# Kernel tuning notes

Measured on AMD Instinct MI355X. Metric: run time of the kernel, lower is better.

Reference implementation:

```python
import jax, jax.numpy as jnp
import numpy as np
import math

B, S, H, NH = 8, 1024, 1024, 16
DH = H // NH


def _ln(x, g, b, eps=1e-5):
    m = x.mean(-1, keepdims=True)
    v = ((x - m) ** 2).mean(-1, keepdims=True)
    return (x - m) / jnp.sqrt(v + eps) * g + b


def _attn(qx, kx, vx, wq, bq, wk, bk, wv, bv, wo, bo, mask):
    b = qx.shape[0]
    def heads(t, w, bias):
        return (t @ w + bias).reshape(b, -1, NH, DH).transpose(0, 2, 1, 3)
    q, k, v = heads(qx, wq, bq), heads(kx, wk, bk), heads(vx, wv, bv)
    corr = jnp.einsum('bhqd,bhkd->bhqk', q, k) / math.sqrt(DH)  # [B,NH,Sq,Sk]
    corr = jnp.where(mask[:, None, :, None] == 0, -1e9, corr)  # mask per query row
    p = jax.nn.softmax(corr, axis=-1)
    o = jnp.einsum('bhqk,bhkd->bhqd', p, v).transpose(0, 2, 1, 3).reshape(b, -1, H)
    return o @ wo + bo


def setup_inputs() -> dict:
    key = jax.random.key(0)
    ks = jax.random.split(key, 16)
    d = {}
    d['x'] = jax.random.normal(ks[0], (B, S, H), jnp.float32)
    d['h'] = jax.random.normal(ks[1], (B, S, H), jnp.float32)
    d['mask'] = jnp.ones((B, S), jnp.int32)
    wnames = ['sa_wq', 'sa_wk', 'sa_wv', 'sa_wo', 'ca_wq', 'ca_wk', 'ca_wv', 'ca_wo', 'ff_w1', 'ff_w2']
    for i, n in enumerate(wnames):
        d[n] = jax.random.normal(ks[2 + i], (H, H), jnp.float32) * 0.02
    for n in ['sa_bq', 'sa_bk', 'sa_bv', 'sa_bo', 'ca_bq', 'ca_bk', 'ca_bv', 'ca_bo', 'ff_b1', 'ff_b2']:
        d[n] = jnp.zeros((H,), jnp.float32)
    for n in ['ln1', 'ln2', 'ln3', 'lnh', 'ff_ln']:
        d[n + '_g'] = jnp.ones((H,), jnp.float32)
        d[n + '_b'] = jnp.zeros((H,), jnp.float32)
    return d


def reference(x, h, mask, ln1_g, ln1_b, ln2_g, ln2_b, ln3_g, ln3_b, lnh_g, lnh_b,
              sa_wq, sa_bq, sa_wk, sa_bk, sa_wv, sa_bv, sa_wo, sa_bo,
              ca_wq, ca_bq, ca_wk, ca_bk, ca_wv, ca_bv, ca_wo, ca_bo,
              ff_w1, ff_b1, ff_w2, ff_b2, ff_ln_g, ff_ln_b):
    # self-attention block (pre-LN, residual)
    xn = _ln(x, ln1_g, ln1_b)
    hidden_in = _attn(xn, xn, xn, sa_wq, sa_bq, sa_wk, sa_bk, sa_wv, sa_bv, sa_wo, sa_bo, mask) + x
    # cross-attention block
    mid_n = _ln(hidden_in, ln2_g, ln2_b)
    hn = _ln(h, lnh_g, lnh_b)
    hidden_mid = _attn(mid_n, hn, hn, ca_wq, ca_bq, ca_wk, ca_bk, ca_wv, ca_bv, ca_wo, ca_bo, mask) + hidden_in
    # position-wise FFN (Conv1d k=1 == pointwise linear) with its own LN+residual
    y = _ln(hidden_mid, ln3_g, ln3_b)
    ff = jax.nn.relu(y @ ff_w1 + ff_b1) @ ff_w2 + ff_b2
    ffo = _ln(ff + y, ff_ln_g, ff_ln_b)
    return ffo + hidden_mid
```

## Files before the change

kernel.cpp:

```cpp
#include <hip/hip_runtime.h>

typedef unsigned short u16;
typedef unsigned int u32;
typedef float f32x4 __attribute__((ext_vector_type(4)));
typedef float f32x16 __attribute__((ext_vector_type(16)));
typedef __bf16 bf16x8 __attribute__((ext_vector_type(8)));

#define MFMA16(a, b, c) __builtin_amdgcn_mfma_f32_16x16x32_bf16(a, b, c, 0, 0, 0)
#define MFMA32(a, b, c) __builtin_amdgcn_mfma_f32_32x32x16_bf16(a, b, c, 0, 0, 0)
#define PLSWAP(x, y) asm volatile("v_permlane32_swap_b32 %0, %1" : "+v"(x), "+v"(y))
#define CFENCE() asm volatile("" ::: "memory")
#define BAR()                         \
    {                                 \
        CFENCE();                     \
        __builtin_amdgcn_s_barrier(); \
        CFENCE();                     \
    }
#define WAITV(n) asm volatile("s_waitcnt vmcnt(" #n ")" ::: "memory")

__device__ __forceinline__ u16 f2b(float f) {
    u32 u = __builtin_bit_cast(u32, f);
    u += 0x7fffu + ((u >> 16) & 1u);
    return (u16)(u >> 16);
}

__device__ __forceinline__ u32 pk2(float a, float b) {
    union { u32 u; __bf16 h[2]; } r;
    r.h[0] = (__bf16)a; r.h[1] = (__bf16)b;
    return r.u;
}

__device__ __forceinline__ void gload16(const u16* g, u16* l) {
    __builtin_amdgcn_global_load_lds((const __attribute__((address_space(1))) void*)g,
                                     (__attribute__((address_space(3))) void*)l, 16, 0, 0);
}

struct W10 { const float* p[10]; };
__global__ __launch_bounds__(256) void tcvt_k(W10 wp, u16* __restrict__ WT0) {
    const float* __restrict__ Wm = wp.p[blockIdx.z];
    u16* __restrict__ WT = WT0 + (size_t)blockIdx.z * 1048576;
    __shared__ float t[32][33];
    int bx = blockIdx.x, by = blockIdx.y;
    int tx = threadIdx.x, ty = threadIdx.y;
#pragma unroll
    for (int j = 0; j < 32; j += 8)
        t[ty + j][tx] = Wm[(size_t)(by * 32 + ty + j) * 1024 + bx * 32 + tx];
    __syncthreads();
#pragma unroll
    for (int j = 0; j < 32; j += 8)
        WT[(size_t)(bx * 32 + ty + j) * 1024 + by * 32 + tx] = f2b(t[tx][ty + j]);
}

__global__ __launch_bounds__(256) void vtr_k(const u16* __restrict__ Vg, int ldv, u16* __restrict__ VT) {
    __shared__ u16 t[32][34];
    int bx = blockIdx.x, by = blockIdx.y, b = blockIdx.z;
    int tx = threadIdx.x, ty = threadIdx.y;
#pragma unroll
    for (int j = 0; j < 32; j += 8)
        t[ty + j][tx] = Vg[(size_t)(b * 1024 + by * 32 + ty + j) * ldv + bx * 32 + tx];
    __syncthreads();
#pragma unroll
    for (int j = 0; j < 32; j += 8)
        VT[(size_t)(b * 1024 + bx * 32 + ty + j) * 1024 + by * 32 + tx] = t[tx][ty + j];
}

template <int MODE>
__global__ __launch_bounds__(256) void ln_k(const float* __restrict__ in1, const float* __restrict__ in2,
                                            const float* __restrict__ gg, const float* __restrict__ bb,
                                            const float* __restrict__ post,
                                            float* __restrict__ of, u16* __restrict__ ob) {
    int row = blockIdx.x, tid = threadIdx.x;
    size_t base = (size_t)row * 1024 + tid * 4;
    float4 x = *(const float4*)(in1 + base);
    if constexpr (MODE & 1) {
        float4 x2 = *(const float4*)(in2 + base);
        x.x += x2.x; x.y += x2.y; x.z += x2.z; x.w += x2.w;
    }
    float s1 = x.x + x.y + x.z + x.w;
    float s2 = x.x * x.x + x.y * x.y + x.z * x.z + x.w * x.w;
#pragma unroll
    for (int m = 32; m >= 1; m >>= 1) { s1 += __shfl_xor(s1, m); s2 += __shfl_xor(s2, m); }
    __shared__ float r1[4], r2[4];
    int lane = tid & 63, w = tid >> 6;
    if (lane == 0) { r1[w] = s1; r2[w] = s2; }
    __syncthreads();
    s1 = r1[0] + r1[1] + r1[2] + r1[3];
    s2 = r2[0] + r2[1] + r2[2] + r2[3];
    float mean = s1 * (1.0f / 1024.0f);
    float var = s2 * (1.0f / 1024.0f) - mean * mean;
    float rstd = rsqrtf(var + 1e-5f);
    float4 gv = *(const float4*)(gg + tid * 4);
    float4 bv = *(const float4*)(bb + tid * 4);
    float y0 = (x.x - mean) * rstd * gv.x + bv.x;
    float y1 = (x.y - mean) * rstd * gv.y + bv.y;
    float y2 = (x.z - mean) * rstd * gv.z + bv.z;
    float y3 = (x.w - mean) * rstd * gv.w + bv.w;
    if constexpr (MODE & 2) {
        float o0 = y0, o1 = y1, o2 = y2, o3 = y3;
        if constexpr (MODE & 8) {
            float4 p = *(const float4*)(post + base);
            o0 += p.x; o1 += p.y; o2 += p.z; o3 += p.w;
        }
        float4 o; o.x = o0; o.y = o1; o.z = o2; o.w = o3;
        *(float4*)(of + base) = o;
    }
    if constexpr (MODE & 4) {
        uint2 pk;
        pk.x = (u32)f2b(y0) | ((u32)f2b(y1) << 16);
        pk.y = (u32)f2b(y2) | ((u32)f2b(y3) << 16);
        *(uint2*)(ob + base) = pk;
    }
}

template <int EPI, int NBT>
__global__ __launch_bounds__(256, 2) void gemm_k(const u16* __restrict__ A, int lda,
                                                 const u16* __restrict__ WT,
                                                 const float* __restrict__ b0, const float* __restrict__ b1,
                                                 const float* __restrict__ b2,
                                                 float sc0, float sc1, float sc2,
                                                 const float* __restrict__ res,
                                                 void* __restrict__ outp, int ldc) {
    __shared__ u16 lds[32768];
    int id = blockIdx.x;
    const int CPX = 64 * NBT / 8;
    int swz = (id & 7) * CPX + (id >> 3);
    int bm = swz / NBT, bn = swz % NBT;
    const int m0 = bm * 128, n0 = bn * 128;
    int tid = threadIdx.x, lane = tid & 63, w = tid >> 6;
    int wm = w >> 1, wn = w & 1;
    int col = lane & 15, fg = lane >> 4;

    int r = tid >> 2, g = tid & 3;
    int gr = r ^ ((r >> 3) & 1);
    int gg = g ^ ((r >> 1) & 3);
    const u16* Asrc = A + (size_t)(m0 + gr) * lda + gg * 8;
    const u16* Bsrc = WT + (size_t)(n0 + gr) * 1024 + gg * 8;
    u16* aDst = lds + w * 512;
    u16* bDst = lds + 16384 + w * 512;

#define STG(slot, kt)                                                      \
    {                                                                      \
        gload16(Asrc + (kt) * 32, aDst + (slot) * 4096);                   \
        gload16(Asrc + (kt) * 32 + (size_t)64 * lda, aDst + (slot) * 4096 + 2048); \
        gload16(Bsrc + (kt) * 32, bDst + (slot) * 4096);                   \
        gload16(Bsrc + (kt) * 32 + (size_t)64 * 1024, bDst + (slot) * 4096 + 2048); \
    }

    int aoff = (((wm * 64 + col) * 32) + fg * 8) ^ ((col >> 1) << 3);
    int boff = (((wn * 64 + col) * 32) + fg * 8) ^ ((col >> 1) << 3);

    f32x4 acc[4][4];
#pragma unroll
    for (int m = 0; m < 4; m++)
#pragma unroll
        for (int n = 0; n < 4; n++) acc[m][n] = (f32x4){0.f, 0.f, 0.f, 0.f};

    auto body = [&](int slot) {
        const u16* aS = lds + slot * 4096;
        const u16* bS = lds + 16384 + slot * 4096;
        bf16x8 af[4], bfv[4];
#pragma unroll
        for (int m = 0; m < 4; m++) af[m] = *(const bf16x8*)(aS + aoff + m * 512);
#pragma unroll
        for (int n = 0; n < 4; n++) bfv[n] = *(const bf16x8*)(bS + boff + n * 512);
        __builtin_amdgcn_s_setprio(1);
#pragma unroll
        for (int m = 0; m < 4; m++)
#pragma unroll
            for (int n = 0; n < 4; n++) acc[m][n] = MFMA16(af[m], bfv[n], acc[m][n]);
        __builtin_amdgcn_s_setprio(0);
    };

    STG(0, 0); STG(1, 1); STG(2, 2);
#pragma unroll 4
    for (int s = 0; s < 29; ++s) {
        STG((s + 3) & 3, s + 3);
        WAITV(12);
        BAR();
        body(s & 3);
        BAR();
    }
    WAITV(8);  BAR(); body(1); BAR();
    WAITV(4);  BAR(); body(2); BAR();
    WAITV(0);  BAR(); body(3); BAR();
#undef STG

    int seg = n0 >> 10;
    const float* bp = (NBT == 8) ? b0 : (seg == 0 ? b0 : (seg == 1 ? b1 : b2));
    float sg = (NBT == 8) ? sc0 : (seg == 0 ? sc0 : (seg == 1 ? sc1 : sc2));
    int nseg = n0 & 1023;
    float bv[4];
#pragma unroll
    for (int n = 0; n < 4; n++) bv[n] = bp[nseg + wn * 64 + n * 16 + col];
#pragma unroll
    for (int m = 0; m < 4; m++) {
#pragma unroll
        for (int rr = 0; rr < 4; rr++) {
            int row = m0 + wm * 64 + m * 16 + fg * 4 + rr;
#pragma unroll
            for (int n = 0; n < 4; n++) {
                int c = n0 + wn * 64 + n * 16 + col;
                size_t idx = (size_t)row * ldc + c;
                float v = (acc[m][n][rr] + bv[n]) * sg;
                if constexpr (EPI == 0) ((u16*)outp)[idx] = f2b(v);
                else if constexpr (EPI == 1) ((u16*)outp)[idx] = f2b(fmaxf(v, 0.f));
                else if constexpr (EPI == 2) ((float*)outp)[idx] = v + res[idx];
            }
        }
    }
}

__global__ __launch_bounds__(256) void attn_k(const u16* __restrict__ Q, int ldq,
                                              const u16* __restrict__ Kc, int ldk,
                                              const u16* __restrict__ VT,
                                              const int* __restrict__ mask,
                                              u16* __restrict__ O, int ldo) {
    const int S = 1024;
    int gid = blockIdx.x;
    int bq = gid >> 7, hh = (gid >> 3) & 15, bb = gid & 7;
    int tid = threadIdx.x, lane = tid & 63, w = tid >> 6;
    int q = lane & 31, hl = lane >> 5;
    int q0w = bq * 128 + w * 32;

    __shared__ u16 sm[18432];
#define KT(b, r, c) sm[(b) * 9216 + (r) * 72 + (c)]
#define VTL(b, r, c) sm[(b) * 9216 + 4608 + (r) * 72 + (c)]

    const u16* Qrow = Q + ((size_t)bb * S + q0w + q) * ldq + hh * 64;
    bool mneg = (mask[bb * S + q0w + q] == 0);
    bf16x8 qf[4];
#pragma unroll
    for (int c = 0; c < 4; c++) {
        qf[c] = *(const bf16x8*)(Qrow + c * 16 + hl * 8);
        if (mneg) qf[c] = (bf16x8)(__bf16)0.f;
    }

    float l = 0.f;
    f32x16 oa[2];
#pragma unroll
    for (int i = 0; i < 16; i++) { oa[0][i] = 0.f; oa[1][i] = 0.f; }

    int kk = tid >> 2, ks = tid & 3;
    const u16* gK = Kc + ((size_t)bb * S + kk) * ldk + hh * 64 + ks * 16;
    const u16* gVT = VT + ((size_t)(bb * 16 + hh) * 64 + kk) * 1024 + ks * 16;
    uint4 kr0, kr1, vr0, vr1;

#define LOADT(t)                                                      \
    {                                                                 \
        const u16* pk_ = gK + (size_t)(t) * 64 * ldk;                 \
        kr0 = *(const uint4*)pk_; kr1 = *(const uint4*)(pk_ + 8);     \
        const u16* pv_ = gVT + (size_t)(t) * 64;                      \
        vr0 = *(const uint4*)pv_; vr1 = *(const uint4*)(pv_ + 8);     \
    }
#define STORET(bf)                                       \
    {                                                    \
        *(uint4*)&KT(bf, kk, ks * 16) = kr0;             \
        *(uint4*)&KT(bf, kk, ks * 16 + 8) = kr1;         \
        *(uint4*)&VTL(bf, kk, ks * 16) = vr0;            \
        *(uint4*)&VTL(bf, kk, ks * 16 + 8) = vr1;        \
    }

    LOADT(0);
    STORET(0);

    for (int t = 0; t < 16; ++t) {
        int cur = t & 1;
        if (t < 15) LOADT(t + 1);
        __syncthreads();

        f32x16 sc[2];
#pragma unroll
        for (int i = 0; i < 16; i++) { sc[0][i] = 0.f; sc[1][i] = 0.f; }
        __builtin_amdgcn_s_setprio(1);
#pragma unroll
        for (int st = 0; st < 2; st++)
#pragma unroll
            for (int c = 0; c < 4; c++) {
                bf16x8 kf = *(const bf16x8*)&KT(cur, st * 32 + q, c * 16 + hl * 8);
                sc[st] = MFMA32(kf, qf[c], sc[st]);
            }
        __builtin_amdgcn_s_setprio(0);

#pragma unroll
        for (int st = 0; st < 2; st++)
#pragma unroll
            for (int rr = 0; rr < 16; rr++) sc[st][rr] = exp2f(sc[st][rr]);
        float ts[8];
#pragma unroll
        for (int i = 0; i < 8; i++)
            ts[i] = (sc[0][i] + sc[0][i + 8]) + (sc[1][i] + sc[1][i + 8]);
#pragma unroll
        for (int i = 0; i < 4; i++) ts[i] += ts[i + 4];
        float rs = (ts[0] + ts[2]) + (ts[1] + ts[3]);
        rs += __shfl_xor(rs, 32);
        l += rs;

        __builtin_amdgcn_s_setprio(1);
#pragma unroll
        for (int st = 0; st < 2; st++) {
            u32 wv[8];
#pragma unroll
            for (int j = 0; j < 8; j++) wv[j] = pk2(sc[st][2 * j], sc[st][2 * j + 1]);
            PLSWAP(wv[0], wv[2]); PLSWAP(wv[1], wv[3]);
            PLSWAP(wv[4], wv[6]); PLSWAP(wv[5], wv[7]);
#pragma unroll
            for (int c = 0; c < 2; c++) {
                union { u32 u[4]; bf16x8 v; } pb;
                pb.u[0] = wv[c * 4 + 0]; pb.u[1] = wv[c * 4 + 1];
                pb.u[2] = wv[c * 4 + 2]; pb.u[3] = wv[c * 4 + 3];
#pragma unroll
                for (int dd = 0; dd < 2; dd++) {
                    bf16x8 vf = *(const bf16x8*)&VTL(cur, dd * 32 + q, st * 32 + c * 16 + hl * 8);
                    oa[dd] = MFMA32(vf, pb.v, oa[dd]);
                }
            }
        }
        __builtin_amdgcn_s_setprio(0);

        if (t < 15) STORET(cur ^ 1);
    }

    __syncthreads();
    float inv = 1.0f / l;
    u16* otw = sm + w * 2304;
#pragma unroll
    for (int dd = 0; dd < 2; dd++)
#pragma unroll
        for (int rr = 0; rr < 16; rr++) {
            int d = (rr & 3) + 8 * (rr >> 2) + 4 * hl + 32 * dd;
            otw[q * 72 + d] = f2b(oa[dd][rr] * inv);
        }
    __syncthreads();
    size_t obase = ((size_t)bb * S + q0w) * ldo + hh * 64;
#pragma unroll
    for (int i = 0; i < 4; i++) {
        int row = i * 8 + (lane >> 3);
        uint4 vdat = *(const uint4*)&otw[row * 72 + (lane & 7) * 8];
        *(uint4*)(O + obase + (size_t)row * ldo + (lane & 7) * 8) = vdat;
    }
#undef KT
#undef VTL
#undef LOADT
#undef STORET
}

extern "C" void kernel_launch(void* const* d_in, const int* in_sizes, int n_in,
                              void* d_out, int out_size, void* d_ws, size_t ws_size,
                              hipStream_t stream) {
    (void)in_sizes; (void)n_in; (void)out_size; (void)ws_size;
    const float* x = (const float*)d_in[0];
    const float* h = (const float*)d_in[1];
    const int* mask = (const int*)d_in[2];
    const float* W[10];
    const float* Bv[10];
    for (int i = 0; i < 10; i++) { W[i] = (const float*)d_in[3 + i]; Bv[i] = (const float*)d_in[13 + i]; }
    const float *ln1g = (const float*)d_in[23], *ln1b = (const float*)d_in[24];
    const float *ln2g = (const float*)d_in[25], *ln2b = (const float*)d_in[26];
    const float *ln3g = (const float*)d_in[27], *ln3b = (const float*)d_in[28];
    const float *lnhg = (const float*)d_in[29], *lnhb = (const float*)d_in[30];
    const float *flng = (const float*)d_in[31], *flnb = (const float*)d_in[32];

    const float SCLE = 0.18033688011112042f;

    char* ws = (char*)d_ws;
    size_t off = 0;
    auto alloc = [&](size_t bytes) -> char* {
        char* p = ws + off;
        off += (bytes + 255) & ~(size_t)255;
        return p;
    };
    const size_t MT = (size_t)8192 * 1024;
    u16* wtb = (u16*)alloc((size_t)10 * 1048576 * 2);
    u16* wt[10];
    for (int i = 0; i < 10; i++) wt[i] = wtb + (size_t)i * 1048576;
    u16* qkv = (u16*)alloc((size_t)8192 * 3072 * 2);
    u16* kv = qkv;
    u16* kb = qkv + (size_t)8192 * 2048;
    u16* bufA = (u16*)alloc(MT * 2);
    u16* qb   = (u16*)alloc(MT * 2);
    float* hid_in  = (float*)alloc(MT * 4);
    float* hid_mid = (float*)alloc(MT * 4);
    float* yf      = (float*)alloc(MT * 4);
    u16* hn = (u16*)yf;
    u16* vt_sa = bufA;
    u16* vt_ca = (u16*)hid_mid;
    float* outF = (float*)d_out;

    W10 wp;
    for (int i = 0; i < 10; i++) wp.p[i] = W[i];
    tcvt_k<<<dim3(32, 32, 10), dim3(32, 8), 0, stream>>>(wp, wtb);

    ln_k<4><<<8192, 256, 0, stream>>>(x, nullptr, ln1g, ln1b, nullptr, nullptr, bufA);
    gemm_k<0, 24><<<1536, 256, 0, stream>>>(bufA, 1024, wt[0], Bv[0], Bv[1], Bv[2], SCLE, 1.f, 1.f, nullptr, qkv, 3072);
    vtr_k<<<dim3(32, 32, 8), dim3(32, 8), 0, stream>>>(qkv + 2048, 3072, vt_sa);
    attn_k<<<1024, 256, 0, stream>>>(qkv, 3072, qkv + 1024, 3072, vt_sa, mask, qkv, 3072);
    gemm_k<2, 8><<<512, 256, 0, stream>>>(qkv, 3072, wt[3], Bv[3], Bv[3], Bv[3], 1.f, 1.f, 1.f, x, hid_in, 1024);

    ln_k<4><<<8192, 256, 0, stream>>>(hid_in, nullptr, ln2g, ln2b, nullptr, nullptr, bufA);
    ln_k<4><<<8192, 256, 0, stream>>>(h, nullptr, lnhg, lnhb, nullptr, nullptr, hn);
    gemm_k<0, 8><<<512, 256, 0, stream>>>(bufA, 1024, wt[4], Bv[4], Bv[4], Bv[4], SCLE, 1.f, 1.f, nullptr, qb, 1024);
    gemm_k<0, 16><<<1024, 256, 0, stream>>>(hn, 1024, wt[5], Bv[5], Bv[6], Bv[6], 1.f, 1.f, 1.f, nullptr, kv, 2048);
    vtr_k<<<dim3(32, 32, 8), dim3(32, 8), 0, stream>>>(kv + 1024, 2048, vt_ca);
    attn_k<<<1024, 256, 0, stream>>>(qb, 1024, kv, 2048, vt_ca, mask, qb, 1024);
    gemm_k<2, 8><<<512, 256, 0, stream>>>(qb, 1024, wt[7], Bv[7], Bv[7], Bv[7], 1.f, 1.f, 1.f, hid_in, hid_mid, 1024);

    ln_k<6><<<8192, 256, 0, stream>>>(hid_mid, nullptr, ln3g, ln3b, nullptr, yf, bufA);
    gemm_k<1, 8><<<512, 256, 0, stream>>>(bufA, 1024, wt[8], Bv[8], Bv[8], Bv[8], 1.f, 1.f, 1.f, nullptr, kb, 1024);
    gemm_k<2, 8><<<512, 256, 0, stream>>>(kb, 1024, wt[9], Bv[9], Bv[9], Bv[9], 1.f, 1.f, 1.f, yf, hid_in, 1024);
    ln_k<10><<<8192, 256, 0, stream>>>(hid_in, nullptr, flng, flnb, hid_mid, outF, nullptr);
}
```

Before: 511.9 us.

## Enlarge GEMM tiles to 256-row blocks with 8 waves and split-phase pipeline

Reworks the GEMM kernel to use 512-thread workgroups with 256xN tiles (N = 256 or 128 chosen per call), 3-slot LDS buffering, and loads for the next stage interleaved between two MFMA half-phases. Larger tiles raise arithmetic intensity and cut global/L2 traffic per FLOP, and grid sizes shrink accordingly. In exchange occupancy drops to one large block per CU, grids of 256 blocks may leave CUs underused on a 256-CU part, and the hand-placed waitcnt counts must match the load pattern exactly.

```diff
diff --git a/kernel.cpp b/kernel.cpp
--- a/kernel.cpp
+++ b/kernel.cpp
@@ -112,94 +112,135 @@
     }
 }
 
-template <int EPI, int NBT>
-__global__ __launch_bounds__(256, 2) void gemm_k(const u16* __restrict__ A, int lda,
-                                                 const u16* __restrict__ WT,
-                                                 const float* __restrict__ b0, const float* __restrict__ b1,
-                                                 const float* __restrict__ b2,
-                                                 float sc0, float sc1, float sc2,
-                                                 const float* __restrict__ res,
-                                                 void* __restrict__ outp, int ldc) {
-    __shared__ u16 lds[32768];
+template <int EPI, int WN, int NBN>
+__global__ __launch_bounds__(512) void gemm_k(const u16* __restrict__ A, int lda,
+                                              const u16* __restrict__ WT,
+                                              const float* __restrict__ b0, const float* __restrict__ b1,
+                                              const float* __restrict__ b2,
+                                              float sc0, float sc1, float sc2,
+                                              const float* __restrict__ res,
+                                              void* __restrict__ outp, int ldc) {
+    constexpr int ASZ = 8192;
+    constexpr int BSZ = (WN == 4) ? 8192 : 4096;
+    constexpr int SLOT = ASZ + BSZ;
+    constexpr int MR = (WN == 4) ? 8 : 4;
+    constexpr int WRS = (WN == 4) ? 128 : 64;
+    constexpr int UN = (WN == 4) ? 4 : 3;
+    __shared__ u16 lds[3 * SLOT];
+    u16* ldsb = &lds[0];
+
     int id = blockIdx.x;
-    const int CPX = 64 * NBT / 8;
+    constexpr int NWG = 32 * NBN;
+    constexpr int CPX = NWG / 8;
     int swz = (id & 7) * CPX + (id >> 3);
-    int bm = swz / NBT, bn = swz % NBT;
-    const int m0 = bm * 128, n0 = bn * 128;
+    int bm = swz / NBN, bn = swz % NBN;
+    const int m0 = bm * 256, n0 = bn * (WN * 64);
     int tid = threadIdx.x, lane = tid & 63, w = tid >> 6;
-    int wm = w >> 1, wn = w & 1;
     int col = lane & 15, fg = lane >> 4;
+    int wr = (WN == 4) ? (w >> 2) : (w >> 1);
+    int wc = w & (WN - 1);
+
+    int swzL = ((col * 32) + fg * 8) ^ ((col >> 1) << 3);
+    int aoff0 = wr * WRS * 32 + swzL;
+    int boff0 = ASZ + wc * 64 * 32 + swzL;
 
     int r = tid >> 2, g = tid & 3;
     int gr = r ^ ((r >> 3) & 1);
-    int gg = g ^ ((r >> 1) & 3);
-    const u16* Asrc = A + (size_t)(m0 + gr) * lda + gg * 8;
-    const u16* Bsrc = WT + (size_t)(n0 + gr) * 1024 + gg * 8;
-    u16* aDst = lds + w * 512;
-    u16* bDst = lds + 16384 + w * 512;
-
-#define STG(slot, kt)                                                      \
-    {                                                                      \
-        gload16(Asrc + (kt) * 32, aDst + (slot) * 4096);                   \
-        gload16(Asrc + (kt) * 32 + (size_t)64 * lda, aDst + (slot) * 4096 + 2048); \
-        gload16(Bsrc + (kt) * 32, bDst + (slot) * 4096);                   \
-        gload16(Bsrc + (kt) * 32 + (size_t)64 * 1024, bDst + (slot) * 4096 + 2048); \
-    }
-
-    int aoff = (((wm * 64 + col) * 32) + fg * 8) ^ ((col >> 1) << 3);
-    int boff = (((wn * 64 + col) * 32) + fg * 8) ^ ((col >> 1) << 3);
-
-    f32x4 acc[4][4];
-#pragma unroll
-    for (int m = 0; m < 4; m++)
+    int gc = g ^ ((r >> 1) & 3);
+    const u16* pA = A + (size_t)(m0 + gr) * lda + gc * 8;
+    const u16* pB = WT + (size_t)(n0 + gr) * 1024 + gc * 8;
+
+#define STGA(t2, snO)                                                                 \
+    {                                                                                 \
+        gload16(pA + (size_t)(t2) * 32, ldsb + (snO) + w * 512);                      \
+        gload16(pA + (size_t)(t2) * 32 + (size_t)128 * lda, ldsb + (snO) + 4096 + w * 512); \
+    }
+#define STGB(t2, snO)                                                                 \
+    {                                                                                 \
+        gload16(pB + (size_t)(t2) * 32, ldsb + (snO) + ASZ + w * 512);                \
+        if constexpr (WN == 4) {                                                      \
+            gload16(pB + (size_t)(t2) * 32 + (size_t)128 * 1024, ldsb + (snO) + ASZ + 4096 + w * 512); \
+        }                                                                             \
+    }
+
+    f32x4 acc[MR][4];
+#pragma unroll
+    for (int m = 0; m < MR; m++)
 #pragma unroll
         for (int n = 0; n < 4; n++) acc[m][n] = (f32x4){0.f, 0.f, 0.f, 0.f};
 
-    auto body = [&](int slot) {
-        const u16* aS = lds + slot * 4096;
-        const u16* bS = lds + 16384 + slot * 4096;
-        bf16x8 af[4], bfv[4];
-#pragma unroll
-        for (int m = 0; m < 4; m++) af[m] = *(const bf16x8*)(aS + aoff + m * 512);
-#pragma unroll
-        for (int n = 0; n < 4; n++) bfv[n] = *(const bf16x8*)(bS + boff + n * 512);
+    STGA(0, 0); STGB(0, 0);
+    STGA(1, SLOT); STGB(1, SLOT);
+    if constexpr (WN == 4) { WAITV(4); } else { WAITV(3); }
+    BAR();
+
+    int sc = 0, sn = 2;
+    for (int t = 0; t < 32; ++t) {
+        int sCur = sc * SLOT, sNxt = sn * SLOT;
+        bf16x8 a0[4], bfv[WN];
+#pragma unroll
+        for (int m = 0; m < 4; m++) a0[m] = *(const bf16x8*)&ldsb[sCur + aoff0 + m * 512];
+#pragma unroll
+        for (int n = 0; n < WN; n++) bfv[n] = *(const bf16x8*)&ldsb[sCur + boff0 + n * 512];
+        if (t < 30) STGA(t + 2, sNxt);
+        BAR();
         __builtin_amdgcn_s_setprio(1);
 #pragma unroll
         for (int m = 0; m < 4; m++)
 #pragma unroll
-            for (int n = 0; n < 4; n++) acc[m][n] = MFMA16(af[m], bfv[n], acc[m][n]);
+            for (int n = 0; n < WN; n++) acc[m][n] = MFMA16(a0[m], bfv[n], acc[m][n]);
         __builtin_amdgcn_s_setprio(0);
-    };
-
-    STG(0, 0); STG(1, 1); STG(2, 2);
-#pragma unroll 4
-    for (int s = 0; s < 29; ++s) {
-        STG((s + 3) & 3, s + 3);
-        WAITV(12);
         BAR();
-        body(s & 3);
-        BAR();
-    }
-    WAITV(8);  BAR(); body(1); BAR();
-    WAITV(4);  BAR(); body(2); BAR();
-    WAITV(0);  BAR(); body(3); BAR();
-#undef STG
+        if constexpr (WN == 4) {
+            bf16x8 a1[4];
+#pragma unroll
+            for (int m = 0; m < 4; m++) a1[m] = *(const bf16x8*)&ldsb[sCur + aoff0 + (m + 4) * 512];
+            if (t < 30) STGB(t + 2, sNxt);
+            BAR();
+            __builtin_amdgcn_s_setprio(1);
+#pragma unroll
+            for (int m = 0; m < 4; m++)
+#pragma unroll
+                for (int n = 0; n < 4; n++) acc[m + 4][n] = MFMA16(a1[m], bfv[n], acc[m + 4][n]);
+            __builtin_amdgcn_s_setprio(0);
+            if (t < 30) { WAITV(4); } else if (t == 30) { WAITV(0); }
+            BAR();
+        } else {
+            bf16x8 b2[2];
+#pragma unroll
+            for (int n = 0; n < 2; n++) b2[n] = *(const bf16x8*)&ldsb[sCur + boff0 + (n + 2) * 512];
+            if (t < 30) STGB(t + 2, sNxt);
+            BAR();
+            __builtin_amdgcn_s_setprio(1);
+#pragma unroll
+            for (int m = 0; m < 4; m++)
+#pragma unroll
+                for (int n = 0; n < 2; n++) acc[m][n + 2] = MFMA16(a0[m], b2[n], acc[m][n + 2]);
+            __builtin_amdgcn_s_setprio(0);
+            if (t < 30) { WAITV(3); } else if (t == 30) { WAITV(0); }
+            BAR();
+        }
+        sc = (sc == 2) ? 0 : sc + 1;
+        sn = (sn == 2) ? 0 : sn + 1;
+    }
+#undef STGA
+#undef STGB
 
     int seg = n0 >> 10;
-    const float* bp = (NBT == 8) ? b0 : (seg == 0 ? b0 : (seg == 1 ? b1 : b2));
-    float sg = (NBT == 8) ? sc0 : (seg == 0 ? sc0 : (seg == 1 ? sc1 : sc2));
+    const float* bp = (seg == 0) ? b0 : (seg == 1 ? b1 : b2);
+    float sg = (seg == 0) ? sc0 : (seg == 1 ? sc1 : sc2);
     int nseg = n0 & 1023;
     float bv[4];
 #pragma unroll
-    for (int n = 0; n < 4; n++) bv[n] = bp[nseg + wn * 64 + n * 16 + col];
-#pragma unroll
-    for (int m = 0; m < 4; m++) {
+    for (int n = 0; n < 4; n++) bv[n] = bp[nseg + wc * 64 + n * 16 + col];
+#pragma unroll
+    for (int m = 0; m < MR; m++) {
 #pragma unroll
         for (int rr = 0; rr < 4; rr++) {
-            int row = m0 + wm * 64 + m * 16 + fg * 4 + rr;
+            int row = m0 + wr * WRS + m * 16 + fg * 4 + rr;
 #pragma unroll
             for (int n = 0; n < 4; n++) {
-                int c = n0 + wn * 64 + n * 16 + col;
+                int c = n0 + wc * 64 + n * 16 + col;
                 size_t idx = (size_t)row * ldc + c;
                 float v = (acc[m][n][rr] + bv[n]) * sg;
                 if constexpr (EPI == 0) ((u16*)outp)[idx] = f2b(v);
@@ -391,21 +432,21 @@
     tcvt_k<<<dim3(32, 32, 10), dim3(32, 8), 0, stream>>>(wp, wtb);
 
     ln_k<4><<<8192, 256, 0, stream>>>(x, nullptr, ln1g, ln1b, nullptr, nullptr, bufA);
-    gemm_k<0, 24><<<1536, 256, 0, stream>>>(bufA, 1024, wt[0], Bv[0], Bv[1], Bv[2], SCLE, 1.f, 1.f, nullptr, qkv, 3072);
+    gemm_k<0, 4, 12><<<384, 512, 0, stream>>>(bufA, 1024, wt[0], Bv[0], Bv[1], Bv[2], SCLE, 1.f, 1.f, nullptr, qkv, 3072);
     vtr_k<<<dim3(32, 32, 8), dim3(32, 8), 0, stream>>>(qkv + 2048, 3072, vt_sa);
     attn_k<<<1024, 256, 0, stream>>>(qkv, 3072, qkv + 1024, 3072, vt_sa, mask, qkv, 3072);
-    gemm_k<2, 8><<<512, 256, 0, stream>>>(qkv, 3072, wt[3], Bv[3], Bv[3], Bv[3], 1.f, 1.f, 1.f, x, hid_in, 1024);
+    gemm_k<2, 2, 8><<<256, 512, 0, stream>>>(qkv, 3072, wt[3], Bv[3], Bv[3], Bv[3], 1.f, 1.f, 1.f, x, hid_in, 1024);
 
     ln_k<4><<<8192, 256, 0, stream>>>(hid_in, nullptr, ln2g, ln2b, nullptr, nullptr, bufA);
     ln_k<4><<<8192, 256, 0, stream>>>(h, nullptr, lnhg, lnhb, nullptr, nullptr, hn);
-    gemm_k<0, 8><<<512, 256, 0, stream>>>(bufA, 1024, wt[4], Bv[4], Bv[4], Bv[4], SCLE, 1.f, 1.f, nullptr, qb, 1024);
-    gemm_k<0, 16><<<1024, 256, 0, stream>>>(hn, 1024, wt[5], Bv[5], Bv[6], Bv[6], 1.f, 1.f, 1.f, nullptr, kv, 2048);
+    gemm_k<0, 2, 8><<<256, 512, 0, stream>>>(bufA, 1024, wt[4], Bv[4], Bv[4], Bv[4], SCLE, 1.f, 1.f, nullptr, qb, 1024);
+    gemm_k<0, 4, 8><<<256, 512, 0, stream>>>(hn, 1024, wt[5], Bv[5], Bv[6], Bv[6], 1.f, 1.f, 1.f, nullptr, kv, 2048);
     vtr_k<<<dim3(32, 32, 8), dim3(32, 8), 0, stream>>>(kv + 1024, 2048, vt_ca);
     attn_k<<<1024, 256, 0, stream>>>(qb, 1024, kv, 2048, vt_ca, mask, qb, 1024);
-    gemm_k<2, 8><<<512, 256, 0, stream>>>(qb, 1024, wt[7], Bv[7], Bv[7], Bv[7], 1.f, 1.f, 1.f, hid_in, hid_mid, 1024);
+    gemm_k<2, 2, 8><<<256, 512, 0, stream>>>(qb, 1024, wt[7], Bv[7], Bv[7], Bv[7], 1.f, 1.f, 1.f, hid_in, hid_mid, 1024);
 
     ln_k<6><<<8192, 256, 0, stream>>>(hid_mid, nullptr, ln3g, ln3b, nullptr, yf, bufA);
-    gemm_k<1, 8><<<512, 256, 0, stream>>>(bufA, 1024, wt[8], Bv[8], Bv[8], Bv[8], 1.f, 1.f, 1.f, nullptr, kb, 1024);
-    gemm_k<2, 8><<<512, 256, 0, stream>>>(kb, 1024, wt[9], Bv[9], Bv[9], Bv[9], 1.f, 1.f, 1.f, yf, hid_in, 1024);
+    gemm_k<1, 2, 8><<<256, 512, 0, stream>>>(bufA, 1024, wt[8], Bv[8], Bv[8], Bv[8], 1.f, 1.f, 1.f, nullptr, kb, 1024);
+    gemm_k<2, 2, 8><<<256, 512, 0, stream>>>(kb, 1024, wt[9], Bv[9], Bv[9], Bv[9], 1.f, 1.f, 1.f, yf, hid_in, 1024);
     ln_k<10><<<8192, 256, 0, stream>>>(hid_in, nullptr, flng, flnb, hid_mid, outF, nullptr);
 }
```

After: 466.3 us. -8.9%, faster.
